# Kernel tuning notes

Hardware: AMD Instinct MI355X
Metric: run time of the kernel (lower is better)

## Reference

```python
import jax, jax.numpy as jnp
import numpy as np

NUM_HEADS = 16
D_KV = 64
NUM_BUCKETS = 32
MAX_DISTANCE = 128


def _relative_position_bucket(rel_pos, num_buckets=NUM_BUCKETS, max_distance=MAX_DISTANCE):
    # bidirectional bucketing (dec_or_not=False -> b_di=True in source)
    nb = num_buckets // 2
    buckets = (rel_pos > 0).astype(jnp.int32) * nb
    rel = jnp.abs(rel_pos)
    max_exact = nb // 2
    is_small = rel < max_exact
    # guard log(0); masked out by is_small anyway
    rel_if_large = max_exact + (
        jnp.log(jnp.maximum(rel, 1).astype(jnp.float32) / max_exact)
        / np.log(max_distance / max_exact) * (nb - max_exact)
    ).astype(jnp.int32)
    rel_if_large = jnp.minimum(rel_if_large, nb - 1)
    return buckets + jnp.where(is_small, rel, rel_if_large)


def setup_inputs() -> dict:
    key = jax.random.key(0)
    ks = jax.random.split(key, 6)
    B, S, D = 2, 2048, 1024
    s = 1.0 / np.sqrt(D)
    return {
        "hidden_states": jax.random.normal(ks[0], (B, S, D), jnp.float32),
        "Wq": jax.random.normal(ks[1], (D, NUM_HEADS * D_KV), jnp.float32) * s,
        "Wk": jax.random.normal(ks[2], (D, NUM_HEADS * D_KV), jnp.float32) * s,
        "Wv": jax.random.normal(ks[3], (D, NUM_HEADS * D_KV), jnp.float32) * s,
        "Wo": jax.random.normal(ks[4], (NUM_HEADS * D_KV, D), jnp.float32) * s,
        "rel_emb": jax.random.normal(ks[5], (NUM_BUCKETS, NUM_HEADS), jnp.float32),
    }


def reference(hidden_states, Wq, Wk, Wv, Wo, rel_emb):
    B, S, D = hidden_states.shape
    H, Dh = NUM_HEADS, D_KV

    def heads(x):  # [B,S,H*Dh] -> [B,H,S,Dh]
        return x.reshape(B, S, H, Dh).transpose(0, 2, 1, 3)

    q = heads(hidden_states @ Wq)
    k = heads(hidden_states @ Wk)
    v = heads(hidden_states @ Wv)

    # T5 attention: no 1/sqrt(d) scaling
    scores = jnp.einsum("bhqd,bhkd->bhqk", q, k)

    # relative position bias (bias_cal)
    pos = jnp.arange(S)
    rel_pos = pos[None, :] - pos[:, None]  # [S_q, S_k]
    buckets = _relative_position_bucket(rel_pos)
    bias = rel_emb[buckets]                       # [S,S,H]
    bias = bias.transpose(2, 0, 1)[None]          # [1,H,S,S]

    scores = scores + bias
    attn = jax.nn.softmax(scores.astype(jnp.float32), axis=-1).astype(scores.dtype)
    # dropout p=0 in eval -> identity
    out = jnp.einsum("bhqk,bhkd->bhqd", attn, v)
    out = out.transpose(0, 2, 1, 3).reshape(B, S, H * Dh)
    return out @ Wo
```

## Files before the change

kernel.cpp:

```cpp
#include <hip/hip_runtime.h>

typedef __bf16 bf16x8 __attribute__((ext_vector_type(8)));
typedef float f32x4 __attribute__((ext_vector_type(4)));

#define LDK 72
#define LOG2E 1.44269504088896f

__device__ __forceinline__ unsigned short bfbits(float x) {
  __bf16 h = (__bf16)x;
  return __builtin_bit_cast(unsigned short, h);
}

__device__ __forceinline__ void gload_lds16(const unsigned short* g, unsigned short* l) {
  __builtin_amdgcn_global_load_lds(
      (const __attribute__((address_space(1))) unsigned int*)(const void*)g,
      (__attribute__((address_space(3))) unsigned int*)(void*)l, 16, 0, 0);
}

__global__ __launch_bounds__(256)
void prelude_kernel(const float* __restrict__ hidden, unsigned short* __restrict__ hid_bf,
                    const float* __restrict__ W0, const float* __restrict__ W1,
                    const float* __restrict__ W2, const float* __restrict__ W3,
                    unsigned short* __restrict__ T0, unsigned short* __restrict__ T1,
                    unsigned short* __restrict__ T2, unsigned short* __restrict__ T3,
                    const float* __restrict__ rel_emb, float* __restrict__ bias_tab) {
  __shared__ __align__(16) unsigned short Tlds[64 * 68];
  const int bx = blockIdx.x, tid = threadIdx.x;
  if (bx < 2048) {
    int idx = (bx * 256 + tid) * 8;
    float4 v0 = *(const float4*)(hidden + idx);
    float4 v1 = *(const float4*)(hidden + idx + 4);
    unsigned short o[8] = {bfbits(v0.x), bfbits(v0.y), bfbits(v0.z), bfbits(v0.w),
                           bfbits(v1.x), bfbits(v1.y), bfbits(v1.z), bfbits(v1.w)};
    *(uint4*)(hid_bf + idx) = *(const uint4*)o;
  } else if (bx < 3072) {
    int flat = bx - 2048;
    int mz = flat >> 8;
    int k0 = ((flat >> 4) & 15) * 64, n0 = (flat & 15) * 64;
    const float* W = mz == 0 ? W0 : (mz == 1 ? W1 : (mz == 2 ? W2 : W3));
    unsigned short* T = mz == 0 ? T0 : (mz == 1 ? T1 : (mz == 2 ? T2 : T3));
#pragma unroll
    for (int p = 0; p < 4; ++p) {
      int idx = p * 256 + tid;
      int kk = idx >> 4, nc = idx & 15;
      float4 v = *(const float4*)(W + (size_t)(k0 + kk) * 1024 + n0 + nc * 4);
      ushort4 s;
      s.x = bfbits(v.x); s.y = bfbits(v.y); s.z = bfbits(v.z); s.w = bfbits(v.w);
      *(ushort4*)(Tlds + kk * 68 + nc * 4) = s;
    }
    __syncthreads();
#pragma unroll
    for (int p = 0; p < 2; ++p) {
      int idx = p * 256 + tid;
      int n = idx >> 3, c = idx & 7;
      unsigned short tmp[8];
#pragma unroll
      for (int j = 0; j < 8; ++j) tmp[j] = Tlds[(c * 8 + j) * 68 + n];
      *(uint4*)(T + (size_t)(n0 + n) * 1024 + k0 + c * 8) = *(const uint4*)tmp;
    }
  } else {
    int i = (bx - 3072) * 256 + tid;
    int h = i >> 12;
    int idx = i & 4095;
    int rp = idx - 2048;
    int base = (rp > 0) ? 16 : 0;
    int rel = rp < 0 ? -rp : rp;
    int b;
    if (rel < 8) {
      b = rel;
    } else {
      b = 8 + (int)(log2f((float)rel * 0.125f) * 2.0f);
      if (b > 15) b = 15;
    }
    bias_tab[h * 4096 + idx] = rel_emb[(base + b) * 16 + h] * LOG2E - 64.0f;
  }
}

template <bool OUT_F32, int BN>
__global__ __launch_bounds__(256)
void gemm_kernel(const unsigned short* __restrict__ A,
                 const unsigned short* __restrict__ Wt0,
                 const unsigned short* __restrict__ Wt1,
                 const unsigned short* __restrict__ Wt2,
                 void* __restrict__ O0v, void* __restrict__ O1v, void* __restrict__ O2v,
                 float scale0) {
  constexpr int NBLK = 1024 / BN;
  constexpr int NT = BN / 32;
  __shared__ __align__(16) unsigned short Alds[128 * 64];
  __shared__ __align__(16) unsigned short Wlds[BN * 64];
  const int tid = threadIdx.x;
  const int which = blockIdx.x / NBLK;
  const int n0 = (blockIdx.x % NBLK) * BN;
  const int m0 = blockIdx.y * 128;
  const unsigned short* Wt = which == 0 ? Wt0 : (which == 1 ? Wt1 : Wt2);
  void* Ov = which == 0 ? O0v : (which == 1 ? O1v : O2v);
  const int wave = tid >> 6, lane = tid & 63, quad = lane >> 4, col = lane & 15;
  const int wm = (wave >> 1) * 64, wn = (wave & 1) * (BN / 2);
  const int wbase = tid & ~63;
  const int sw = col & 7;

  f32x4 acc[4][NT] = {};

  for (int kt = 0; kt < 16; ++kt) {
    const int k0 = kt * 64;
    __syncthreads();
#pragma unroll
    for (int p = 0; p < 4; ++p) {
      int idx = p * 256 + tid;
      int m = idx >> 3, c = idx & 7;
      int cs = c ^ (m & 7);
      gload_lds16(A + (size_t)(m0 + m) * 1024 + k0 + cs * 8,
                  Alds + (size_t)(p * 256 + wbase) * 8);
    }
#pragma unroll
    for (int p = 0; p < BN / 32; ++p) {
      int idx = p * 256 + tid;
      int n = idx >> 3, c = idx & 7;
      int cs = c ^ (n & 7);
      gload_lds16(Wt + (size_t)(n0 + n) * 1024 + k0 + cs * 8,
                  Wlds + (size_t)(p * 256 + wbase) * 8);
    }
    __syncthreads();
#pragma unroll
    for (int ks = 0; ks < 2; ++ks) {
      bf16x8 af[4], wf[NT];
#pragma unroll
      for (int mt = 0; mt < 4; ++mt)
        af[mt] = *(const bf16x8*)(Alds + (wm + mt * 16 + col) * 64 +
                                  (((ks * 4 + quad) ^ sw) * 8));
#pragma unroll
      for (int nt = 0; nt < NT; ++nt)
        wf[nt] = *(const bf16x8*)(Wlds + (wn + nt * 16 + col) * 64 +
                                  (((ks * 4 + quad) ^ sw) * 8));
#pragma unroll
      for (int mt = 0; mt < 4; ++mt)
#pragma unroll
        for (int nt = 0; nt < NT; ++nt)
          acc[mt][nt] = __builtin_amdgcn_mfma_f32_16x16x32_bf16(af[mt], wf[nt], acc[mt][nt], 0, 0, 0);
    }
  }
  if (!OUT_F32 && which == 2) {
    unsigned short* Ot = (unsigned short*)Ov;
#pragma unroll
    for (int nt = 0; nt < NT; ++nt)
#pragma unroll
      for (int mt = 0; mt < 4; ++mt) {
        int n = n0 + wn + nt * 16 + col;
        int m = m0 + wm + mt * 16 + quad * 4;
        ushort4 s;
        s.x = bfbits(acc[mt][nt][0]); s.y = bfbits(acc[mt][nt][1]);
        s.z = bfbits(acc[mt][nt][2]); s.w = bfbits(acc[mt][nt][3]);
        *(ushort4*)(Ot + (size_t)n * 4096 + m) = s;
      }
  } else {
    const float sc = (which == 0) ? scale0 : 1.0f;
#pragma unroll
    for (int mt = 0; mt < 4; ++mt)
#pragma unroll
      for (int nt = 0; nt < NT; ++nt)
#pragma unroll
        for (int r = 0; r < 4; ++r) {
          int m = m0 + wm + mt * 16 + quad * 4 + r;
          int n = n0 + wn + nt * 16 + col;
          float x = acc[mt][nt][r] * sc;
          if (OUT_F32)
            ((float*)Ov)[(size_t)m * 1024 + n] = x;
          else
            ((unsigned short*)Ov)[(size_t)m * 1024 + n] = bfbits(x);
        }
  }
}

__global__ __launch_bounds__(256)
void attn_kernel(unsigned short* __restrict__ q_ws,
                 const unsigned short* __restrict__ k_ws,
                 const unsigned short* __restrict__ vt_ws,
                 const float* __restrict__ bias_tab) {
  __shared__ __align__(16) unsigned short Klds[2][64 * 64];
  __shared__ __align__(16) unsigned short Vlds[2][64 * 64];
  __shared__ __align__(16) unsigned short Plds[128 * LDK];
  __shared__ float bias_lds[2][192];
  __shared__ float l_sh[128];
  const int tid = threadIdx.x;
  const int q0 = blockIdx.x * 128;
  const int bh = blockIdx.y;
  const int b = bh >> 4, h = bh & 15;
  const int wave = tid >> 6, lane = tid & 63, quad = lane >> 4, col = lane & 15;
  const int wbase = tid & ~63;
  const int sw = col & 7;

  bf16x8 qf[2][2];
#pragma unroll
  for (int nt = 0; nt < 2; ++nt) {
    size_t row = (size_t)(b * 2048 + q0 + wave * 32 + nt * 16 + col) * 1024 + h * 64;
    qf[nt][0] = *(const bf16x8*)(q_ws + row + quad * 8);
    qf[nt][1] = *(const bf16x8*)(q_ws + row + 32 + quad * 8);
  }
  const float bias_far_pos = bias_tab[h * 4096 + 2048 + 512];
  const float bias_far_neg = bias_tab[h * 4096 + 2048 - 512];

  float l_lane[2] = {0.f, 0.f};
  f32x4 of[2][4] = {};

  auto stage = [&](int kt, int buf) {
    const int k0 = kt * 64;
#pragma unroll
    for (int p = 0; p < 2; ++p) {
      int idx = p * 256 + tid;
      int key = idx >> 3, c = idx & 7;
      int cs = c ^ (key & 7);
      gload_lds16(k_ws + (size_t)(b * 2048 + k0 + key) * 1024 + h * 64 + cs * 8,
                  Klds[buf] + (size_t)(p * 256 + wbase) * 8);
    }
#pragma unroll
    for (int p = 0; p < 2; ++p) {
      int idx = p * 256 + tid;
      int d = idx >> 3, c = idx & 7;
      int cs = c ^ (d & 7);
      gload_lds16(vt_ws + (size_t)(h * 64 + d) * 4096 + b * 2048 + k0 + cs * 8,
                  Vlds[buf] + (size_t)(p * 256 + wbase) * 8);
    }
    const int diff = k0 - q0;
    const bool farr = (diff >= 256) || (diff <= -192);
    if (!farr && tid < 191)
      bias_lds[buf][tid] = bias_tab[h * 4096 + 2048 + k0 - q0 - 127 + tid];
  };

  stage(0, 0);

  for (int kt = 0; kt < 32; ++kt) {
    const int cur = kt & 1;
    const int k0 = kt * 64;
    const int diff = k0 - q0;
    const bool far = (diff >= 256) || (diff <= -192);
    __syncthreads();
    if (kt + 1 < 32) stage(kt + 1, cur ^ 1);

    f32x4 st[4][2];
    if (far) {
      const float c0 = (diff > 0) ? bias_far_pos : bias_far_neg;
#pragma unroll
      for (int mt = 0; mt < 4; ++mt)
#pragma unroll
        for (int nt = 0; nt < 2; ++nt)
#pragma unroll
          for (int r = 0; r < 4; ++r) st[mt][nt][r] = c0;
    } else {
#pragma unroll
      for (int mt = 0; mt < 4; ++mt)
#pragma unroll
        for (int nt = 0; nt < 2; ++nt)
#pragma unroll
          for (int r = 0; r < 4; ++r)
            st[mt][nt][r] =
                bias_lds[cur][(mt * 16 + quad * 4 + r) - (wave * 32 + nt * 16 + col) + 127];
    }
#pragma unroll
    for (int ks = 0; ks < 2; ++ks)
#pragma unroll
      for (int mt = 0; mt < 4; ++mt) {
        bf16x8 kf = *(const bf16x8*)(Klds[cur] + (mt * 16 + col) * 64 +
                                     (((ks * 4 + quad) ^ sw) * 8));
        st[mt][0] = __builtin_amdgcn_mfma_f32_16x16x32_bf16(kf, qf[0][ks], st[mt][0], 0, 0, 0);
        st[mt][1] = __builtin_amdgcn_mfma_f32_16x16x32_bf16(kf, qf[1][ks], st[mt][1], 0, 0, 0);
      }

#pragma unroll
    for (int nt = 0; nt < 2; ++nt)
#pragma unroll
      for (int mt = 0; mt < 4; ++mt) {
        float p0 = __builtin_amdgcn_exp2f(st[mt][nt][0]);
        float p1 = __builtin_amdgcn_exp2f(st[mt][nt][1]);
        float p2 = __builtin_amdgcn_exp2f(st[mt][nt][2]);
        float p3 = __builtin_amdgcn_exp2f(st[mt][nt][3]);
        l_lane[nt] += (p0 + p1) + (p2 + p3);
        ushort4 pk;
        pk.x = bfbits(p0); pk.y = bfbits(p1); pk.z = bfbits(p2); pk.w = bfbits(p3);
        *(ushort4*)(Plds + (wave * 32 + nt * 16 + col) * LDK + mt * 16 + quad * 4) = pk;
      }
    __threadfence_block();

#pragma unroll
    for (int ks = 0; ks < 2; ++ks) {
      bf16x8 pf0 = *(const bf16x8*)(Plds + (wave * 32 + col) * LDK + ks * 32 + quad * 8);
      bf16x8 pf1 = *(const bf16x8*)(Plds + (wave * 32 + 16 + col) * LDK + ks * 32 + quad * 8);
#pragma unroll
      for (int dn = 0; dn < 4; ++dn) {
        bf16x8 vf = *(const bf16x8*)(Vlds[cur] + (dn * 16 + col) * 64 +
                                     (((ks * 4 + quad) ^ sw) * 8));
        of[0][dn] = __builtin_amdgcn_mfma_f32_16x16x32_bf16(pf0, vf, of[0][dn], 0, 0, 0);
        of[1][dn] = __builtin_amdgcn_mfma_f32_16x16x32_bf16(pf1, vf, of[1][dn], 0, 0, 0);
      }
    }
  }

#pragma unroll
  for (int nt = 0; nt < 2; ++nt) {
    l_lane[nt] += __shfl_xor(l_lane[nt], 16, 64);
    l_lane[nt] += __shfl_xor(l_lane[nt], 32, 64);
  }
  l_sh[wave * 32 + col] = l_lane[0];
  l_sh[wave * 32 + 16 + col] = l_lane[1];
  __syncthreads();
#pragma unroll
  for (int mtp = 0; mtp < 2; ++mtp)
#pragma unroll
    for (int r = 0; r < 4; ++r) {
      float inv = 1.0f / fmaxf(l_sh[wave * 32 + mtp * 16 + quad * 4 + r], 1e-30f);
      size_t row = (size_t)(b * 2048 + q0 + wave * 32 + mtp * 16 + quad * 4 + r);
#pragma unroll
      for (int dn = 0; dn < 4; ++dn)
        q_ws[row * 1024 + h * 64 + dn * 16 + col] = bfbits(of[mtp][dn][r] * inv);
    }
}

extern "C" void kernel_launch(void* const* d_in, const int* in_sizes, int n_in,
                              void* d_out, int out_size, void* d_ws, size_t ws_size,
                              hipStream_t stream) {
  const float* hidden = (const float*)d_in[0];
  const float* Wq = (const float*)d_in[1];
  const float* Wk = (const float*)d_in[2];
  const float* Wv = (const float*)d_in[3];
  const float* Wo = (const float*)d_in[4];
  const float* rel_emb = (const float*)d_in[5];
  float* out = (float*)d_out;

  unsigned short* q_ws = (unsigned short*)d_ws;
  unsigned short* k_ws = q_ws + 4194304;
  unsigned short* vt_ws = k_ws + 4194304;
  unsigned short* wt_q = vt_ws + 4194304;
  unsigned short* wt_k = wt_q + 1048576;
  unsigned short* wt_v = wt_k + 1048576;
  unsigned short* wt_o = wt_v + 1048576;
  float* bias_tab = (float*)(wt_o + 1048576);
  unsigned short* hid_bf = (unsigned short*)d_out;

  prelude_kernel<<<3328, 256, 0, stream>>>(hidden, hid_bf, Wq, Wk, Wv, Wo,
                                           wt_q, wt_k, wt_v, wt_o, rel_emb, bias_tab);
  gemm_kernel<false, 128><<<dim3(24, 32), 256, 0, stream>>>(
      hid_bf, wt_q, wt_k, wt_v, q_ws, k_ws, vt_ws, LOG2E);
  attn_kernel<<<dim3(16, 32), 256, 0, stream>>>(q_ws, k_ws, vt_ws, bias_tab);
  gemm_kernel<true, 64><<<dim3(16, 32), 256, 0, stream>>>(
      q_ws, wt_o, wt_o, wt_o, out, out, out, 1.0f);
}
```

Measured before the change: 196.8 us.

## Register-prefetch GEMM tiles and compute softmax row sums via MFMA

The GEMM kernel no longer uses direct global-to-LDS loads. It now prefetches the next K-tile into registers while computing on the current tile, then writes the swizzled tile into LDS after the barrier. This aims to overlap global load latency with MFMA work, at the cost of extra VGPRs and explicit LDS stores. Separately, the attention kernel now computes the softmax denominator with an extra MFMA against a vector of ones, using the bf16 P values, instead of per-lane fp32 adds, shuffles and a shared-memory reduction with a barrier.

```diff
diff --git a/kernel.cpp b/kernel.cpp
--- a/kernel.cpp
+++ b/kernel.cpp
@@ -96,31 +96,37 @@
   void* Ov = which == 0 ? O0v : (which == 1 ? O1v : O2v);
   const int wave = tid >> 6, lane = tid & 63, quad = lane >> 4, col = lane & 15;
   const int wm = (wave >> 1) * 64, wn = (wave & 1) * (BN / 2);
-  const int wbase = tid & ~63;
   const int sw = col & 7;
 
   f32x4 acc[4][NT] = {};
+  uint4 pa[4], pw[NT];
+
+  const int am[4] = {(0 * 256 + tid) >> 3, (1 * 256 + tid) >> 3,
+                     (2 * 256 + tid) >> 3, (3 * 256 + tid) >> 3};
+  const int ac = tid & 7;
+
+  auto prefetch = [&](int kt) {
+    const int k0 = kt * 64;
+#pragma unroll
+    for (int p = 0; p < 4; ++p)
+      pa[p] = *(const uint4*)(A + (size_t)(m0 + am[p]) * 1024 + k0 + ac * 8);
+#pragma unroll
+    for (int p = 0; p < NT; ++p)
+      pw[p] = *(const uint4*)(Wt + (size_t)(n0 + am[p]) * 1024 + k0 + ac * 8);
+  };
+
+  prefetch(0);
 
   for (int kt = 0; kt < 16; ++kt) {
-    const int k0 = kt * 64;
     __syncthreads();
 #pragma unroll
-    for (int p = 0; p < 4; ++p) {
-      int idx = p * 256 + tid;
-      int m = idx >> 3, c = idx & 7;
-      int cs = c ^ (m & 7);
-      gload_lds16(A + (size_t)(m0 + m) * 1024 + k0 + cs * 8,
-                  Alds + (size_t)(p * 256 + wbase) * 8);
-    }
-#pragma unroll
-    for (int p = 0; p < BN / 32; ++p) {
-      int idx = p * 256 + tid;
-      int n = idx >> 3, c = idx & 7;
-      int cs = c ^ (n & 7);
-      gload_lds16(Wt + (size_t)(n0 + n) * 1024 + k0 + cs * 8,
-                  Wlds + (size_t)(p * 256 + wbase) * 8);
-    }
+    for (int p = 0; p < 4; ++p)
+      *(uint4*)(Alds + am[p] * 64 + (ac ^ (am[p] & 7)) * 8) = pa[p];
+#pragma unroll
+    for (int p = 0; p < NT; ++p)
+      *(uint4*)(Wlds + am[p] * 64 + (ac ^ (am[p] & 7)) * 8) = pw[p];
     __syncthreads();
+    if (kt + 1 < 16) prefetch(kt + 1);
 #pragma unroll
     for (int ks = 0; ks < 2; ++ks) {
       bf16x8 af[4], wf[NT];
@@ -180,7 +186,6 @@
   __shared__ __align__(16) unsigned short Vlds[2][64 * 64];
   __shared__ __align__(16) unsigned short Plds[128 * LDK];
   __shared__ float bias_lds[2][192];
-  __shared__ float l_sh[128];
   const int tid = threadIdx.x;
   const int q0 = blockIdx.x * 128;
   const int bh = blockIdx.y;
@@ -199,8 +204,12 @@
   const float bias_far_pos = bias_tab[h * 4096 + 2048 + 512];
   const float bias_far_neg = bias_tab[h * 4096 + 2048 - 512];
 
-  float l_lane[2] = {0.f, 0.f};
+  bf16x8 vone;
+#pragma unroll
+  for (int j = 0; j < 8; ++j) vone[j] = (__bf16)1.0f;
+
   f32x4 of[2][4] = {};
+  f32x4 l_acc[2] = {};
 
   auto stage = [&](int kt, int buf) {
     const int k0 = kt * 64;
@@ -273,7 +282,6 @@
         float p1 = __builtin_amdgcn_exp2f(st[mt][nt][1]);
         float p2 = __builtin_amdgcn_exp2f(st[mt][nt][2]);
         float p3 = __builtin_amdgcn_exp2f(st[mt][nt][3]);
-        l_lane[nt] += (p0 + p1) + (p2 + p3);
         ushort4 pk;
         pk.x = bfbits(p0); pk.y = bfbits(p1); pk.z = bfbits(p2); pk.w = bfbits(p3);
         *(ushort4*)(Plds + (wave * 32 + nt * 16 + col) * LDK + mt * 16 + quad * 4) = pk;
@@ -284,6 +292,8 @@
     for (int ks = 0; ks < 2; ++ks) {
       bf16x8 pf0 = *(const bf16x8*)(Plds + (wave * 32 + col) * LDK + ks * 32 + quad * 8);
       bf16x8 pf1 = *(const bf16x8*)(Plds + (wave * 32 + 16 + col) * LDK + ks * 32 + quad * 8);
+      l_acc[0] = __builtin_amdgcn_mfma_f32_16x16x32_bf16(pf0, vone, l_acc[0], 0, 0, 0);
+      l_acc[1] = __builtin_amdgcn_mfma_f32_16x16x32_bf16(pf1, vone, l_acc[1], 0, 0, 0);
 #pragma unroll
       for (int dn = 0; dn < 4; ++dn) {
         bf16x8 vf = *(const bf16x8*)(Vlds[cur] + (dn * 16 + col) * 64 +
@@ -295,18 +305,10 @@
   }
 
 #pragma unroll
-  for (int nt = 0; nt < 2; ++nt) {
-    l_lane[nt] += __shfl_xor(l_lane[nt], 16, 64);
-    l_lane[nt] += __shfl_xor(l_lane[nt], 32, 64);
-  }
-  l_sh[wave * 32 + col] = l_lane[0];
-  l_sh[wave * 32 + 16 + col] = l_lane[1];
-  __syncthreads();
-#pragma unroll
   for (int mtp = 0; mtp < 2; ++mtp)
 #pragma unroll
     for (int r = 0; r < 4; ++r) {
-      float inv = 1.0f / fmaxf(l_sh[wave * 32 + mtp * 16 + quad * 4 + r], 1e-30f);
+      float inv = 1.0f / fmaxf(l_acc[mtp][r], 1e-30f);
       size_t row = (size_t)(b * 2048 + q0 + wave * 32 + mtp * 16 + quad * 4 + r);
 #pragma unroll
       for (int dn = 0; dn < 4; ++dn)
```

Result: slower. 312.0 us (+58.5%).
